# Kernel optimization log

Hardware: AMD Instinct MI355X
Metric: run time of the kernel (lower is better)

The kernel has to match this reference:

```python
import jax, jax.numpy as jnp
import numpy as np

# GCK basis vectors: all palindromic, so convolution == correlation for them.
_V = np.array([[1., 1., 1.], [1., -1., 1.], [1., 1., -1.]], dtype=np.float32)


def _lin_combs(kernels):
    """Coefficients c s.t. each 3x3 kernel = sum_k c_k * (v_i outer v_j), k=i*3+j.
    kernels: (O, C, 3, 3) -> (O, C*9), matching torch linCombs layout."""
    O, C = kernels.shape[0], kernels.shape[1]
    basis_flat = jnp.asarray(np.kron(_V, _V))           # (9, 9), symmetric
    basis_inv = jnp.linalg.inv(basis_flat)              # 9x9, tiny
    w = kernels.reshape(O, C, 9)
    comb = jnp.einsum('kl,ocl->ock', basis_inv, w)      # (O, C, 9)
    return comb.reshape(O, C * 9)


def setup_inputs() -> dict:
    key = jax.random.key(0)
    k1, k2 = jax.random.split(key)
    C_in, C_out, D = 16, 32, 1024
    x = jax.random.normal(k1, (C_in, D + 2, D + 2), dtype=jnp.float32)
    kernels = jax.random.normal(k2, (C_out, C_in, 3, 3), dtype=jnp.float32)
    return {"x": x, "kernels": kernels}


def reference(x, kernels):
    V = jnp.asarray(_V, dtype=x.dtype)
    lin = _lin_combs(kernels)                                   # (O, C*9)
    O = kernels.shape[0]
    C, H, W = x.shape
    D = H - 2  # result_dim (square image)
    # rowwise pass: 3-tap 'box' filters along height -> (C, 3, D, W)
    rw = jnp.stack([x[:, :-2, :], x[:, 1:-1, :], x[:, 2:, :]], axis=0)  # (3, C, D, W)
    rw = jnp.einsum('ir,rchw->cihw', V, rw)                              # (C, 3, D, W)
    # colwise pass: 3-tap filters along width -> (C, 3, 3, D, D)
    cw = jnp.stack([rw[..., :-2], rw[..., 1:-1], rw[..., 2:]], axis=0)   # (3, C, 3, D, D)
    cw = jnp.einsum('js,scihw->cijhw', V, cw)                            # (C, 3, 3, D, D)
    # final per-output-channel linear combination of the 9 basis responses
    cw = cw.reshape(C * 9, D * D)
    out = lin @ cw                                                       # (O, D*D)
    return out.reshape(O, D, D)
```

## Files before the change

### kernel.cpp

```cpp
#include <hip/hip_runtime.h>

typedef __attribute__((ext_vector_type(8))) short short8;
typedef __attribute__((ext_vector_type(16))) float f32x16;
typedef __attribute__((ext_vector_type(2))) float f32x2;
typedef __attribute__((ext_vector_type(2))) unsigned int uint2v;

#define HW 1026
#define CH_STRIDE (HW * HW)
#define TW 32
#define ROW_BYTES 1088
#define X_ROWS 18
#define X_LDS (X_ROWS * ROW_BYTES)
#define W_LDS (9 * 32 * 16 * 2)

__device__ __forceinline__ unsigned short f2bf(float f) {
    unsigned int u = __builtin_bit_cast(unsigned int, f);
    u += 0x7fffu + ((u >> 16) & 1u);
    return (unsigned short)(u >> 16);
}

template<int NROWS>
__device__ __forceinline__ void stage_tile(const float* __restrict__ x, int xrow0, int w0,
                                           int tid, unsigned char* __restrict__ buf) {
    constexpr int UNITS = 4 * NROWS * 17;
    f32x2 vA[4][4], vB[4];
    #pragma unroll
    for (int k = 0; k < 4; ++k) {
        const int idx = tid + k * 256;
        if (idx < UNITS) {
            const int c4  = idx / (NROWS * 17);
            const int rem = idx - c4 * (NROWS * 17);
            const int row = rem / 17;
            const int u   = rem - row * 17;
            const float* base = x + (4 * c4) * CH_STRIDE + (xrow0 + row) * HW + (w0 + 2 * u);
            #pragma unroll
            for (int j = 0; j < 4; ++j)
                vA[k][j] = *(const f32x2*)(base + j * CH_STRIDE);
        }
    }
    {
        const int idx = tid + 4 * 256;
        if (idx < UNITS) {
            const int c4  = idx / (NROWS * 17);
            const int rem = idx - c4 * (NROWS * 17);
            const int row = rem / 17;
            const int u   = rem - row * 17;
            const float* base = x + (4 * c4) * CH_STRIDE + (xrow0 + row) * HW + (w0 + 2 * u);
            #pragma unroll
            for (int j = 0; j < 4; ++j)
                vB[j] = *(const f32x2*)(base + j * CH_STRIDE);
        }
    }
    #pragma unroll
    for (int k = 0; k < 5; ++k) {
        const int idx = tid + k * 256;
        if (idx < UNITS) {
            const int c4  = idx / (NROWS * 17);
            const int rem = idx - c4 * (NROWS * 17);
            const int row = rem / 17;
            const int u   = rem - row * 17;
            #pragma unroll
            for (int p = 0; p < 2; ++p) {
                const int pp = 2 * u + p;
                const f32x2 q0 = (k < 4) ? vA[k & 3][0] : vB[0];
                const f32x2 q1 = (k < 4) ? vA[k & 3][1] : vB[1];
                const f32x2 q2 = (k < 4) ? vA[k & 3][2] : vB[2];
                const f32x2 q3 = (k < 4) ? vA[k & 3][3] : vB[3];
                const unsigned int lo  = (unsigned int)f2bf(q0[p]) |
                                         ((unsigned int)f2bf(q1[p]) << 16);
                const unsigned int hi2 = (unsigned int)f2bf(q2[p]) |
                                         ((unsigned int)f2bf(q3[p]) << 16);
                const int s16 = ((c4 >> 1) ^ (pp >> 2) ^ (pp >> 3)) & 1;
                const int off = row * ROW_BYTES + pp * 32 + s16 * 16 + (c4 & 1) * 8;
                uint2v t; t.x = lo; t.y = hi2;
                *(uint2v*)(buf + off) = t;
            }
        }
    }
}

template<int BASE>
__device__ __forceinline__ void compute_store(const unsigned char* __restrict__ s_x,
                                              const unsigned char* __restrict__ s_w,
                                              float* __restrict__ out,
                                              int h0, int w0, int wv, int n, int hi) {
    short8 af[9];
    #pragma unroll
    for (int rs = 0; rs < 9; ++rs)
        af[rs] = *(const short8*)(s_w + rs * 1024 + n * 32 + hi * 16);

    #pragma unroll
    for (int t = 0; t < 4; ++t) {
        const int baserow = wv * 4 + t;
        f32x16 acc;
        #pragma unroll
        for (int q = 0; q < 16; ++q) acc[q] = 0.0f;
        #pragma unroll
        for (int r = 0; r < 3; ++r) {
            #pragma unroll
            for (int s = 0; s < 3; ++s) {
                int rr = BASE + baserow + r;
                if (rr >= X_ROWS) rr -= X_ROWS;
                const int w   = n + s;
                const int s16 = (hi ^ (w >> 2) ^ (w >> 3)) & 1;
                const int off = rr * ROW_BYTES + w * 32 + s16 * 16;
                const short8 bfr = *(const short8*)(s_x + off);
                acc = __builtin_amdgcn_mfma_f32_32x32x16_bf16(af[r * 3 + s], bfr, acc, 0, 0, 0);
            }
        }
        const int h = h0 + BASE + baserow;
        float* obase = out + (h << 10) + w0 + n;
        #pragma unroll
        for (int q = 0; q < 16; ++q) {
            const int o = (q & 3) + 8 * (q >> 2) + 4 * hi;
            obase[o << 20] = acc[q];
        }
    }
}

__global__ __launch_bounds__(256, 4)
void gck3x3_mfma_kernel(const float* __restrict__ x,
                        const float* __restrict__ kern,
                        float* __restrict__ out) {
    __shared__ __attribute__((aligned(16))) unsigned char s_mem[X_LDS + W_LDS];
    unsigned char* s_x = s_mem;
    unsigned char* s_w = s_mem + X_LDS;

    const int tid  = threadIdx.x;
    const int lane = tid & 63;
    const int wv   = tid >> 6;
    const int n    = lane & 31;
    const int hi   = lane >> 5;

    const int bid = blockIdx.x;
    const int swz = (bid & 7) * 128 + (bid >> 3);
    const int h0  = (swz >> 5) * 32;
    const int w0  = (swz & 31) * TW;

    stage_tile<18>(x, h0, w0, tid, s_x);

    {
        float wreg[18];
        #pragma unroll
        for (int k = 0; k < 18; ++k)
            wreg[k] = kern[tid + 256 * k];
        #pragma unroll
        for (int k = 0; k < 18; ++k) {
            const int idx = tid + 256 * k;
            const int o   = idx / 144;
            const int rm  = idx - o * 144;
            const int c   = rm / 9;
            const int rs  = rm - c * 9;
            *(short*)(s_w + rs * 1024 + o * 32 + c * 2) = (short)f2bf(wreg[k]);
        }
    }
    __syncthreads();

    compute_store<0>(s_x, s_w, out, h0, w0, wv, n, hi);
    __syncthreads();

    stage_tile<16>(x, h0 + 18, w0, tid, s_x);
    __syncthreads();

    compute_store<16>(s_x, s_w, out, h0, w0, wv, n, hi);
}

extern "C" void kernel_launch(void* const* d_in, const int* in_sizes, int n_in,
                              void* d_out, int out_size, void* d_ws, size_t ws_size,
                              hipStream_t stream) {
    (void)in_sizes; (void)n_in; (void)d_ws; (void)ws_size; (void)out_size;
    const float* x    = (const float*)d_in[0];
    const float* kern = (const float*)d_in[1];
    float*       out  = (float*)d_out;
    gck3x3_mfma_kernel<<<1024, 256, 0, stream>>>(x, kern, out);
}
```

Before: 36.78 us.

## Process four row tiles per block with ring-buffered LDS staging

Each block now handles 64 output rows instead of 32. It loops over four 16-row tiles and reuses the 2-row halo in a circular LDS buffer, so the grid shrinks to 512 blocks. This amortizes the weight staging and halo reloads over more output and cuts redundant global reads. In exchange there are fewer blocks to spread over the CUs, the launch bound drops to 2 waves per EU, and the load/compute phases stay serialized by barriers.

```diff
diff --git a/kernel.cpp b/kernel.cpp
--- a/kernel.cpp
+++ b/kernel.cpp
@@ -12,6 +12,7 @@
 #define X_ROWS 18
 #define X_LDS (X_ROWS * ROW_BYTES)
 #define W_LDS (9 * 32 * 16 * 2)
+#define T_TILES 4
 
 __device__ __forceinline__ unsigned short f2bf(float f) {
     unsigned int u = __builtin_bit_cast(unsigned int, f);
@@ -21,7 +22,7 @@
 
 template<int NROWS>
 __device__ __forceinline__ void stage_tile(const float* __restrict__ x, int xrow0, int w0,
-                                           int tid, unsigned char* __restrict__ buf) {
+                                           int tid, unsigned char* __restrict__ buf, int ro) {
     constexpr int UNITS = 4 * NROWS * 17;
     f32x2 vA[4][4], vB[4];
     #pragma unroll
@@ -59,6 +60,8 @@
             const int rem = idx - c4 * (NROWS * 17);
             const int row = rem / 17;
             const int u   = rem - row * 17;
+            int phys = ro + row;
+            if (phys >= X_ROWS) phys -= X_ROWS;
             #pragma unroll
             for (int p = 0; p < 2; ++p) {
                 const int pp = 2 * u + p;
@@ -71,7 +74,7 @@
                 const unsigned int hi2 = (unsigned int)f2bf(q2[p]) |
                                          ((unsigned int)f2bf(q3[p]) << 16);
                 const int s16 = ((c4 >> 1) ^ (pp >> 2) ^ (pp >> 3)) & 1;
-                const int off = row * ROW_BYTES + pp * 32 + s16 * 16 + (c4 & 1) * 8;
+                const int off = phys * ROW_BYTES + pp * 32 + s16 * 16 + (c4 & 1) * 8;
                 uint2v t; t.x = lo; t.y = hi2;
                 *(uint2v*)(buf + off) = t;
             }
@@ -79,11 +82,11 @@
     }
 }
 
-template<int BASE>
 __device__ __forceinline__ void compute_store(const unsigned char* __restrict__ s_x,
                                               const unsigned char* __restrict__ s_w,
                                               float* __restrict__ out,
-                                              int h0, int w0, int wv, int n, int hi) {
+                                              int hout, int w0, int wv, int n, int hi,
+                                              int base) {
     short8 af[9];
     #pragma unroll
     for (int rs = 0; rs < 9; ++rs)
@@ -97,10 +100,10 @@
         for (int q = 0; q < 16; ++q) acc[q] = 0.0f;
         #pragma unroll
         for (int r = 0; r < 3; ++r) {
+            int rr = base + baserow + r;
+            if (rr >= X_ROWS) rr -= X_ROWS;
             #pragma unroll
             for (int s = 0; s < 3; ++s) {
-                int rr = BASE + baserow + r;
-                if (rr >= X_ROWS) rr -= X_ROWS;
                 const int w   = n + s;
                 const int s16 = (hi ^ (w >> 2) ^ (w >> 3)) & 1;
                 const int off = rr * ROW_BYTES + w * 32 + s16 * 16;
@@ -108,7 +111,7 @@
                 acc = __builtin_amdgcn_mfma_f32_32x32x16_bf16(af[r * 3 + s], bfr, acc, 0, 0, 0);
             }
         }
-        const int h = h0 + BASE + baserow;
+        const int h = hout + baserow;
         float* obase = out + (h << 10) + w0 + n;
         #pragma unroll
         for (int q = 0; q < 16; ++q) {
@@ -118,7 +121,7 @@
     }
 }
 
-__global__ __launch_bounds__(256, 4)
+__global__ __launch_bounds__(256, 2)
 void gck3x3_mfma_kernel(const float* __restrict__ x,
                         const float* __restrict__ kern,
                         float* __restrict__ out) {
@@ -133,12 +136,11 @@
     const int hi   = lane >> 5;
 
     const int bid = blockIdx.x;
-    const int swz = (bid & 7) * 128 + (bid >> 3);
-    const int h0  = (swz >> 5) * 32;
+    const int swz = (bid & 7) * 64 + (bid >> 3);
+    const int h0  = (swz >> 5) * (16 * T_TILES);
     const int w0  = (swz & 31) * TW;
 
-    stage_tile<18>(x, h0, w0, tid, s_x);
-
+    stage_tile<18>(x, h0, w0, tid, s_x, 0);
     {
         float wreg[18];
         #pragma unroll
@@ -156,13 +158,23 @@
     }
     __syncthreads();
 
-    compute_store<0>(s_x, s_w, out, h0, w0, wv, n, hi);
-    __syncthreads();
-
-    stage_tile<16>(x, h0 + 18, w0, tid, s_x);
-    __syncthreads();
-
-    compute_store<16>(s_x, s_w, out, h0, w0, wv, n, hi);
+    int base = 0;
+    int ro   = 0;
+    int hout = h0;
+    int xr   = h0 + 18;
+    #pragma unroll 1
+    for (int j = 0; j < T_TILES; ++j) {
+        compute_store(s_x, s_w, out, hout, w0, wv, n, hi, base);
+        if (j + 1 < T_TILES) {
+            __syncthreads();
+            stage_tile<16>(x, xr, w0, tid, s_x, ro);
+            __syncthreads();
+            xr += 16;
+            ro   = (ro + 16 >= X_ROWS) ? ro - 2 : ro + 16;
+            base = (base + 16 >= X_ROWS) ? base - 2 : base + 16;
+            hout += 16;
+        }
+    }
 }
 
 extern "C" void kernel_launch(void* const* d_in, const int* in_sizes, int n_in,
@@ -172,5 +184,5 @@
     const float* x    = (const float*)d_in[0];
     const float* kern = (const float*)d_in[1];
     float*       out  = (float*)d_out;
-    gck3x3_mfma_kernel<<<1024, 256, 0, stream>>>(x, kern, out);
+    gck3x3_mfma_kernel<<<512, 256, 0, stream>>>(x, kern, out);
 }
```

Result: slower. 40.17 us (+9.2%).
